# Optimization experiments

Hardware: AMD Instinct MI355X
Metric: run time of the kernel (lower is better)

The kernel has to match this reference:

```python
import jax, jax.numpy as jnp
import numpy as np

ALPHA, GAMMA = 0.25, 2.0
LOC_CW, CLS_CW, OBJ_CW = 1.0, 0.25, 0.1
LOC_W, CLS_W, OBJ_W = 1.0, 1.0, 1.0
B, K, N, C, D = 128, 2048, 4, 64, 3


def _lsa_rows(cost):
    """Hungarian (Kuhn-Munkres with potentials). cost: [n,m], n<=m.
    Returns col assigned to each row (same optimum as scipy.linear_sum_assignment)."""
    cost = np.asarray(cost, dtype=np.float64)
    n, m = cost.shape
    u = np.zeros(n + 1); v = np.zeros(m + 1)
    p = np.zeros(m + 1, dtype=np.int64)
    way = np.zeros(m + 1, dtype=np.int64)
    for i in range(1, n + 1):
        p[0] = i; j0 = 0
        minv = np.full(m + 1, np.inf)
        used = np.zeros(m + 1, dtype=bool)
        while True:
            used[j0] = True
            i0 = p[j0]
            cur = cost[i0 - 1] - u[i0] - v[1:]
            mv = minv[1:]; wy = way[1:]
            free = ~used[1:]
            upd = free & (cur < mv)
            mv[upd] = cur[upd]; wy[upd] = j0
            jrel = np.where(free)[0]
            j1 = jrel[np.argmin(mv[jrel])] + 1
            delta = mv[j1 - 1]
            uj = np.where(used)[0]
            u[p[uj]] += delta
            v[uj] -= delta
            mv[free] -= delta
            j0 = j1
            if p[j0] == 0:
                break
        while j0:
            j1 = way[j0]; p[j0] = p[j1]; j0 = j1
    col_of_row = np.full(n, -1, dtype=np.int64)
    for j in range(1, m + 1):
        if p[j] > 0:
            col_of_row[p[j] - 1] = j - 1
    return col_of_row


def focal_bce(logits, targets, alpha=ALPHA, gamma=GAMMA):
    p = jax.nn.sigmoid(logits)
    # stable BCE-with-logits
    ce = jnp.maximum(logits, 0.0) - logits * targets + jnp.log1p(jnp.exp(-jnp.abs(logits)))
    p_t = p * targets + (1.0 - p) * (1.0 - targets)
    alpha_t = alpha * targets + (1.0 - alpha) * (1.0 - targets)
    return alpha_t * ce * (1.0 - p_t) ** gamma


def _match(loc_out, obj_logit, cls_logit, gt_loc, gt_cls):
    """Hungarian matching (detached, matches torch no_grad block). Returns pred_idx [B,N];
    gt index n is matched to prediction pred_idx[b,n]."""
    eps = 1e-8
    vp = loc_out / jnp.clip(jnp.linalg.norm(loc_out, axis=-1, keepdims=True), eps)
    vt = gt_loc / jnp.clip(jnp.linalg.norm(gt_loc, axis=-1, keepdims=True), eps)
    cos = jnp.clip(jnp.einsum('bkd,bnd->bkn', vp, vt), -1.0 + 1e-6, 1.0 - 1e-6)
    loc_cost = jnp.arccos(cos) / jnp.pi  # [B,K,N]
    # cls cost: focal BCE summed over POSITIVE classes only / pos_count.
    # focal(x, t=1) = alpha * softplus(-x) * (1 - sigmoid(x))**gamma  -> einsum with one-hot gts
    focal_pos = ALPHA * jax.nn.softplus(-cls_logit) * (1.0 - jax.nn.sigmoid(cls_logit)) ** GAMMA  # [B,K,C]
    pos_cnt = jnp.maximum(gt_cls.sum(-1), 1.0)  # [B,N]
    cls_cost = jnp.einsum('bkc,bnc->bkn', focal_pos, gt_cls) / pos_cnt[:, None, :]
    obj_cost = -jax.nn.sigmoid(obj_logit)[:, :, None]  # [B,K,1]
    total = LOC_CW * loc_cost + CLS_CW * cls_cost + OBJ_CW * obj_cost  # [B,K,N]
    total_np = np.asarray(jax.device_get(total))
    # transpose to [N,K] so rows (gt) <= cols (preds)
    pred_idx = np.stack([_lsa_rows(total_np[b].T) for b in range(total_np.shape[0])])
    return jnp.asarray(pred_idx)  # [B,N] int


def _losses(loc_out, obj_logit, cls_logit, gt_loc, gt_cls, pred_idx):
    b, k = loc_out.shape[0], loc_out.shape[1]
    mp_loc = jnp.take_along_axis(loc_out, pred_idx[:, :, None], axis=1)  # [B,N,D]
    mp_cls = jnp.take_along_axis(cls_logit, pred_idx[:, :, None], axis=1)  # [B,N,C]
    # loc criterion = MSE; per-sample mean then /B == global mean (all samples have N>0)
    loc_loss = jnp.mean((mp_loc - gt_loc) ** 2)
    cls_loss = jnp.mean(focal_bce(mp_cls, gt_cls))
    obj_target = jnp.zeros((b, k), dtype=obj_logit.dtype).at[jnp.arange(b)[:, None], pred_idx].set(1.0)
    obj_ce = jnp.maximum(obj_logit, 0.0) - obj_logit * obj_target + jnp.log1p(jnp.exp(-jnp.abs(obj_logit)))
    obj_loss = jnp.mean(obj_ce)
    return LOC_W * loc_loss + CLS_W * cls_loss + OBJ_W * obj_loss


def setup_inputs() -> dict:
    key = jax.random.key(0)
    k1, k2, k3, k4, k5 = jax.random.split(key, 5)
    loc_out = jax.random.normal(k1, (B, K, D), dtype=jnp.float32)
    obj_logit = jax.random.normal(k2, (B, K), dtype=jnp.float32)
    cls_logit = jax.random.normal(k3, (B, K, C), dtype=jnp.float32)
    gt_loc = jax.random.normal(k4, (B, N, D), dtype=jnp.float32)
    cls_idx = jax.random.randint(k5, (B, N), 0, C)
    gt_cls = jax.nn.one_hot(cls_idx, C, dtype=jnp.float32)
    return {'loc_out': loc_out, 'obj_logit': obj_logit, 'cls_logit': cls_logit,
            'gt_loc': gt_loc, 'gt_cls': gt_cls}


def reference(loc_out, obj_logit, cls_logit, gt_loc, gt_cls):
    pred_idx = _match(loc_out, obj_logit, cls_logit, gt_loc, gt_cls)
    return _losses(loc_out, obj_logit, cls_logit, gt_loc, gt_cls, pred_idx)
```

## Files before the change

### kernel.cpp

```cpp
#include <hip/hip_runtime.h>
#include <math.h>
#include <limits.h>

#define BB 128
#define KK 2048
#define NN 4
#define CC 64
#define DD 3
#define SL 8
#define KS (KK/SL)
#define THREADS 256

#define OFF_CVAL 0
#define OFF_CIDX (BB*SL*NN*NN)
#define OFF_OBJ  (2*BB*SL*NN*NN)
#define OFF_PART (OFF_OBJ + BB*SL)

__device__ __forceinline__ float acospi_fast(float x) {
    float ax = fabsf(x);
    float p = ((-0.0187293f*ax + 0.0742610f)*ax - 0.2121144f)*ax + 1.5707288f;
    float r = sqrtf(1.f - ax) * p;
    r = (x >= 0.f) ? r : 3.14159274f - r;
    return r * 0.31830988618379067f;
}

__global__ void __launch_bounds__(THREADS)
crit_cost(const float* __restrict__ loc_out, const float* __restrict__ obj_logit,
          const float* __restrict__ cls_logit, const float* __restrict__ gt_loc,
          const float* __restrict__ gt_cls, float* __restrict__ ws)
{
    __shared__ float cost[NN][KS];
    __shared__ float obj_s[4];

    const int sl  = blockIdx.x;
    const int b   = blockIdx.y;
    const int tid = threadIdx.x;
    const int w   = tid >> 6, lane = tid & 63;
    const int k   = sl*KS + tid;

    const float* lp = loc_out + ((size_t)b*KK + k)*DD;
    float l0 = lp[0], l1 = lp[1], l2 = lp[2];
    float x  = obj_logit[b*KK + k];

    int   cls[NN]; float posin[NN];
    #pragma unroll
    for (int n = 0; n < NN; ++n) {
        float v = gt_cls[(b*NN+n)*CC + lane];
        unsigned long long m = __ballot(v > 0.5f);
        cls[n]   = __ffsll((unsigned long long)m) - 1;
        posin[n] = 1.f / fmaxf((float)__popcll(m), 1.f);
    }

    float z[NN];
    #pragma unroll
    for (int n = 0; n < NN; ++n)
        z[n] = cls_logit[((size_t)b*KK + k)*CC + cls[n]];

    float vt[NN][DD];
    #pragma unroll
    for (int n = 0; n < NN; ++n) {
        float g0 = gt_loc[(b*NN+n)*DD+0];
        float g1 = gt_loc[(b*NN+n)*DD+1];
        float g2 = gt_loc[(b*NN+n)*DD+2];
        float gin = 1.f / fmaxf(sqrtf(g0*g0 + g1*g1 + g2*g2), 1e-8f);
        vt[n][0] = g0*gin; vt[n][1] = g1*gin; vt[n][2] = g2*gin;
    }

    float inv = 1.f / fmaxf(sqrtf(l0*l0 + l1*l1 + l2*l2), 1e-8f);
    float v0 = l0*inv, v1 = l1*inv, v2 = l2*inv;
    float obj_base = fmaxf(x, 0.f) + log1pf(expf(-fabsf(x)));
    float oc = -0.1f / (1.f + __expf(-x));
    #pragma unroll
    for (int n = 0; n < NN; ++n) {
        float cosv = v0*vt[n][0] + v1*vt[n][1] + v2*vt[n][2];
        cosv = fminf(fmaxf(cosv, -1.f + 1e-6f), 1.f - 1e-6f);
        float loc_c = acospi_fast(cosv);
        float zz = z[n];
        float e  = __expf(-fabsf(zz));
        float lg = __logf(1.f + e);
        float sp = (zz >= 0.f) ? lg : (lg - zz);
        float r1 = 1.f / (1.f + e);
        float sn = (zz >= 0.f) ? e*r1 : r1;
        float fp = 0.25f * sp * sn * sn;
        cost[n][tid] = loc_c + 0.25f*fp*posin[n] + oc;
    }

    float osum = obj_base;
    #pragma unroll
    for (int off = 32; off > 0; off >>= 1) osum += __shfl_xor(osum, off, 64);
    if (lane == 0) obj_s[w] = osum;
    __syncthreads();

    float vv[4]; int gi[4];
    #pragma unroll
    for (int j = 0; j < 4; ++j) {
        vv[j] = cost[w][lane + 64*j];
        gi[j] = sl*KS + lane + 64*j;
    }
    float cr_val[NN]; int cr_idx[NN];
    #pragma unroll
    for (int r = 0; r < NN; ++r) {
        float bv = vv[0]; int bi = gi[0];
        #pragma unroll
        for (int j = 1; j < 4; ++j)
            if (vv[j] < bv || (vv[j] == bv && gi[j] < bi)) { bv = vv[j]; bi = gi[j]; }
        #pragma unroll
        for (int off = 32; off > 0; off >>= 1) {
            float ov = __shfl_xor(bv, off, 64);
            int   oi = __shfl_xor(bi, off, 64);
            if (ov < bv || (ov == bv && oi < bi)) { bv = ov; bi = oi; }
        }
        cr_val[r] = bv; cr_idx[r] = bi;
        #pragma unroll
        for (int j = 0; j < 4; ++j) if (gi[j] == bi) vv[j] = INFINITY;
    }
    if (lane == 0) {
        int base = ((b*SL + sl)*NN + w)*NN;
        int* wsi = (int*)ws;
        #pragma unroll
        for (int r = 0; r < NN; ++r) {
            ws[OFF_CVAL + base + r]  = cr_val[r];
            wsi[OFF_CIDX + base + r] = cr_idx[r];
        }
    }
    if (tid == 0)
        ws[OFF_OBJ + b*SL + sl] = obj_s[0] + obj_s[1] + obj_s[2] + obj_s[3];
}

__global__ void __launch_bounds__(THREADS)
crit_match(const float* __restrict__ loc_out, const float* __restrict__ obj_logit,
           const float* __restrict__ cls_logit, const float* __restrict__ gt_loc,
           const float* __restrict__ gt_cls, float* __restrict__ ws)
{
    __shared__ float cand_val[NN][NN];
    __shared__ int   cand_idx[NN][NN];
    __shared__ int   s_pred[NN];
    __shared__ float s_best[4];
    __shared__ int   s_bestc[4];
    __shared__ float red[4];

    const int b = blockIdx.x, tid = threadIdx.x;
    const int w = tid >> 6, lane = tid & 63;
    const int* wsi = (const int*)ws;

    {
        float v = INFINITY; int idx = INT_MAX;
        if (lane < SL*NN) {
            int sl = lane >> 2, r = lane & 3;
            int base = ((b*SL + sl)*NN + w)*NN + r;
            v   = ws[OFF_CVAL + base];
            idx = wsi[OFF_CIDX + base];
        }
        #pragma unroll
        for (int r = 0; r < NN; ++r) {
            float bv = v; int bi = idx;
            #pragma unroll
            for (int off = 32; off > 0; off >>= 1) {
                float ov = __shfl_xor(bv, off, 64);
                int   oi = __shfl_xor(bi, off, 64);
                if (ov < bv || (ov == bv && oi < bi)) { bv = ov; bi = oi; }
            }
            if (lane == 0) { cand_val[w][r] = bv; cand_idx[w][r] = bi; }
            if (idx == bi) v = INFINITY;
        }
    }
    __syncthreads();

    {
        int a0 = (tid >> 6) & 3, a1 = (tid >> 4) & 3, a2 = (tid >> 2) & 3, a3 = tid & 3;
        int c0 = cand_idx[0][a0], c1 = cand_idx[1][a1];
        int c2 = cand_idx[2][a2], c3 = cand_idx[3][a3];
        bool valid = (c0!=c1) & (c0!=c2) & (c0!=c3) & (c1!=c2) & (c1!=c3) & (c2!=c3);
        float t = cand_val[0][a0] + cand_val[1][a1] + cand_val[2][a2] + cand_val[3][a3];
        float bv = valid ? t : INFINITY;
        int   bc = tid;
        #pragma unroll
        for (int off = 32; off > 0; off >>= 1) {
            float ov = __shfl_xor(bv, off, 64);
            int   oc = __shfl_xor(bc, off, 64);
            if (ov < bv || (ov == bv && oc < bc)) { bv = ov; bc = oc; }
        }
        if (lane == 0) { s_best[w] = bv; s_bestc[w] = bc; }
    }
    __syncthreads();

    if (tid == 0) {
        float bv = s_best[0]; int bc = s_bestc[0];
        for (int i = 1; i < 4; ++i)
            if (s_best[i] < bv || (s_best[i] == bv && s_bestc[i] < bc)) { bv = s_best[i]; bc = s_bestc[i]; }
        int a0 = (bc >> 6) & 3, a1 = (bc >> 4) & 3, a2 = (bc >> 2) & 3, a3 = bc & 3;
        s_pred[0] = cand_idx[0][a0]; s_pred[1] = cand_idx[1][a1];
        s_pred[2] = cand_idx[2][a2]; s_pred[3] = cand_idx[3][a3];

        float om = 0.f;
        for (int sl = 0; sl < SL; ++sl) om += ws[OFF_OBJ + b*SL + sl];
        for (int n = 0; n < NN; ++n) om -= obj_logit[b*KK + s_pred[n]];
        ws[OFF_PART + b*3 + 2] = om;

        float s = 0.f;
        for (int n = 0; n < NN; ++n)
            for (int d = 0; d < DD; ++d) {
                float diff = loc_out[((size_t)b*KK + s_pred[n])*DD + d] - gt_loc[(b*NN+n)*DD + d];
                s += diff*diff;
            }
        ws[OFF_PART + b*3 + 0] = s;
    }
    __syncthreads();

    {
        int n = w, c = lane;
        float zz = cls_logit[((size_t)b*KK + s_pred[n])*CC + c];
        float tgt = gt_cls[(b*NN+n)*CC + c];
        float p  = 1.f / (1.f + expf(-zz));
        float ce = fmaxf(zz, 0.f) - zz*tgt + log1pf(expf(-fabsf(zz)));
        float pt = p*tgt + (1.f-p)*(1.f-tgt);
        float at = 0.25f*tgt + 0.75f*(1.f-tgt);
        float om1 = 1.f - pt;
        float r = at * ce * om1 * om1;
        #pragma unroll
        for (int off = 32; off > 0; off >>= 1) r += __shfl_xor(r, off, 64);
        if (lane == 0) red[n] = r;
    }
    __syncthreads();
    if (tid == 0) ws[OFF_PART + b*3 + 1] = red[0] + red[1] + red[2] + red[3];
}

__global__ void __launch_bounds__(BB)
crit_final(const float* __restrict__ ws, float* __restrict__ out)
{
    __shared__ float s2[3][2];
    int t = threadIdx.x;
    int w = t >> 6, lane = t & 63;
    float a = ws[OFF_PART + t*3+0];
    float b = ws[OFF_PART + t*3+1];
    float c = ws[OFF_PART + t*3+2];
    #pragma unroll
    for (int off = 32; off > 0; off >>= 1) {
        a += __shfl_xor(a, off, 64);
        b += __shfl_xor(b, off, 64);
        c += __shfl_xor(c, off, 64);
    }
    if (lane == 0) { s2[0][w] = a; s2[1][w] = b; s2[2][w] = c; }
    __syncthreads();
    if (t == 0) {
        out[0] = (s2[0][0]+s2[0][1]) / (float)(BB*NN*DD)
               + (s2[1][0]+s2[1][1]) / (float)(BB*NN*CC)
               + (s2[2][0]+s2[2][1]) / (float)(BB*KK);
    }
}

extern "C" void kernel_launch(void* const* d_in, const int* in_sizes, int n_in,
                              void* d_out, int out_size, void* d_ws, size_t ws_size,
                              hipStream_t stream) {
    const float* loc_out   = (const float*)d_in[0];
    const float* obj_logit = (const float*)d_in[1];
    const float* cls_logit = (const float*)d_in[2];
    const float* gt_loc    = (const float*)d_in[3];
    const float* gt_cls    = (const float*)d_in[4];
    float* ws  = (float*)d_ws;
    float* out = (float*)d_out;

    hipLaunchKernelGGL(crit_cost, dim3(SL, BB), dim3(THREADS), 0, stream,
                       loc_out, obj_logit, cls_logit, gt_loc, gt_cls, ws);
    hipLaunchKernelGGL(crit_match, dim3(BB), dim3(THREADS), 0, stream,
                       loc_out, obj_logit, cls_logit, gt_loc, gt_cls, ws);
    hipLaunchKernelGGL(crit_final, dim3(1), dim3(BB), 0, stream, ws, out);
}
```

Baseline: 28.39 us.

## Fuse cost and match kernels into one per-batch block kernel

```diff
diff --git a/kernel.cpp b/kernel.cpp
--- a/kernel.cpp
+++ b/kernel.cpp
@@ -7,14 +7,10 @@
 #define NN 4
 #define CC 64
 #define DD 3
-#define SL 8
-#define KS (KK/SL)
-#define THREADS 256
-
-#define OFF_CVAL 0
-#define OFF_CIDX (BB*SL*NN*NN)
-#define OFF_OBJ  (2*BB*SL*NN*NN)
-#define OFF_PART (OFF_OBJ + BB*SL)
+#define TA 512
+#define KPT (KK/TA)
+#define NW (TA/64)
+
 
 __device__ __forceinline__ float acospi_fast(float x) {
     float ax = fabsf(x);
@@ -24,37 +20,43 @@
     return r * 0.31830988618379067f;
 }
 
-__global__ void __launch_bounds__(THREADS)
-crit_cost(const float* __restrict__ loc_out, const float* __restrict__ obj_logit,
-          const float* __restrict__ cls_logit, const float* __restrict__ gt_loc,
-          const float* __restrict__ gt_cls, float* __restrict__ ws)
+__device__ __forceinline__ float cls_term_fast(float zz, float posin) {
+    float e  = __expf(-fabsf(zz));
+    float lg = __logf(1.f + e);
+    float sp = (zz >= 0.f) ? lg : (lg - zz);
+    float r1 = 1.f / (1.f + e);
+    float sn = (zz >= 0.f) ? e*r1 : r1;
+    float fp = 0.25f * sp * sn * sn;
+    return 0.25f * fp * posin;
+}
+
+__global__ void __launch_bounds__(TA)
+crit_all(const float* __restrict__ loc_out, const float* __restrict__ obj_logit,
+         const float* __restrict__ cls_logit, const float* __restrict__ gt_loc,
+         const float* __restrict__ gt_cls, float* __restrict__ ws)
 {
-    __shared__ float cost[NN][KS];
-    __shared__ float obj_s[4];
-
-    const int sl  = blockIdx.x;
-    const int b   = blockIdx.y;
+    __shared__ float wv_val[NW][NN][4];
+    __shared__ int   wv_idx[NW][NN][4];
+    __shared__ float obj_s[NW];
+    __shared__ float cand_val[NN][NN];
+    __shared__ int   cand_idx[NN][NN];
+    __shared__ int   s_pred[NN];
+    __shared__ float s_best[4];
+    __shared__ int   s_bestc[4];
+    __shared__ float red[4];
+
+    const int b   = blockIdx.x;
     const int tid = threadIdx.x;
     const int w   = tid >> 6, lane = tid & 63;
-    const int k   = sl*KS + tid;
-
-    const float* lp = loc_out + ((size_t)b*KK + k)*DD;
-    float l0 = lp[0], l1 = lp[1], l2 = lp[2];
-    float x  = obj_logit[b*KK + k];
 
     int   cls[NN]; float posin[NN];
     #pragma unroll
     for (int n = 0; n < NN; ++n) {
         float v = gt_cls[(b*NN+n)*CC + lane];
         unsigned long long m = __ballot(v > 0.5f);
-        cls[n]   = __ffsll((unsigned long long)m) - 1;
+        cls[n]   = __ffsll(m) - 1;
         posin[n] = 1.f / fmaxf((float)__popcll(m), 1.f);
     }
-
-    float z[NN];
-    #pragma unroll
-    for (int n = 0; n < NN; ++n)
-        z[n] = cls_logit[((size_t)b*KK + k)*CC + cls[n]];
 
     float vt[NN][DD];
     #pragma unroll
@@ -66,93 +68,63 @@
         vt[n][0] = g0*gin; vt[n][1] = g1*gin; vt[n][2] = g2*gin;
     }
 
-    float inv = 1.f / fmaxf(sqrtf(l0*l0 + l1*l1 + l2*l2), 1e-8f);
-    float v0 = l0*inv, v1 = l1*inv, v2 = l2*inv;
-    float obj_base = fmaxf(x, 0.f) + log1pf(expf(-fabsf(x)));
-    float oc = -0.1f / (1.f + __expf(-x));
+    float cost[KPT][NN];
+    float obj_base = 0.f;
+    #pragma unroll
+    for (int j = 0; j < KPT; ++j) {
+        const int k = tid + TA*j;
+        const float* lp = loc_out + ((size_t)b*KK + k)*DD;
+        float l0 = lp[0], l1 = lp[1], l2 = lp[2];
+        float x  = obj_logit[b*KK + k];
+        float inv = 1.f / fmaxf(sqrtf(l0*l0 + l1*l1 + l2*l2), 1e-8f);
+        float v0 = l0*inv, v1 = l1*inv, v2 = l2*inv;
+        obj_base += fmaxf(x, 0.f) + log1pf(expf(-fabsf(x)));
+        float oc = -0.1f / (1.f + __expf(-x));
+        #pragma unroll
+        for (int n = 0; n < NN; ++n) {
+            float cosv = v0*vt[n][0] + v1*vt[n][1] + v2*vt[n][2];
+            cosv = fminf(fmaxf(cosv, -1.f + 1e-6f), 1.f - 1e-6f);
+            float zz = cls_logit[((size_t)b*KK + k)*CC + cls[n]];
+            cost[j][n] = acospi_fast(cosv) + cls_term_fast(zz, posin[n]) + oc;
+        }
+    }
+
+    {
+        float osum = obj_base;
+        #pragma unroll
+        for (int off = 32; off > 0; off >>= 1) osum += __shfl_xor(osum, off, 64);
+        if (lane == 0) obj_s[w] = osum;
+    }
+
     #pragma unroll
     for (int n = 0; n < NN; ++n) {
-        float cosv = v0*vt[n][0] + v1*vt[n][1] + v2*vt[n][2];
-        cosv = fminf(fmaxf(cosv, -1.f + 1e-6f), 1.f - 1e-6f);
-        float loc_c = acospi_fast(cosv);
-        float zz = z[n];
-        float e  = __expf(-fabsf(zz));
-        float lg = __logf(1.f + e);
-        float sp = (zz >= 0.f) ? lg : (lg - zz);
-        float r1 = 1.f / (1.f + e);
-        float sn = (zz >= 0.f) ? e*r1 : r1;
-        float fp = 0.25f * sp * sn * sn;
-        cost[n][tid] = loc_c + 0.25f*fp*posin[n] + oc;
-    }
-
-    float osum = obj_base;
-    #pragma unroll
-    for (int off = 32; off > 0; off >>= 1) osum += __shfl_xor(osum, off, 64);
-    if (lane == 0) obj_s[w] = osum;
-    __syncthreads();
-
-    float vv[4]; int gi[4];
-    #pragma unroll
-    for (int j = 0; j < 4; ++j) {
-        vv[j] = cost[w][lane + 64*j];
-        gi[j] = sl*KS + lane + 64*j;
-    }
-    float cr_val[NN]; int cr_idx[NN];
-    #pragma unroll
-    for (int r = 0; r < NN; ++r) {
-        float bv = vv[0]; int bi = gi[0];
-        #pragma unroll
-        for (int j = 1; j < 4; ++j)
-            if (vv[j] < bv || (vv[j] == bv && gi[j] < bi)) { bv = vv[j]; bi = gi[j]; }
-        #pragma unroll
-        for (int off = 32; off > 0; off >>= 1) {
-            float ov = __shfl_xor(bv, off, 64);
-            int   oi = __shfl_xor(bi, off, 64);
-            if (ov < bv || (ov == bv && oi < bi)) { bv = ov; bi = oi; }
-        }
-        cr_val[r] = bv; cr_idx[r] = bi;
-        #pragma unroll
-        for (int j = 0; j < 4; ++j) if (gi[j] == bi) vv[j] = INFINITY;
-    }
-    if (lane == 0) {
-        int base = ((b*SL + sl)*NN + w)*NN;
-        int* wsi = (int*)ws;
-        #pragma unroll
-        for (int r = 0; r < NN; ++r) {
-            ws[OFF_CVAL + base + r]  = cr_val[r];
-            wsi[OFF_CIDX + base + r] = cr_idx[r];
-        }
-    }
-    if (tid == 0)
-        ws[OFF_OBJ + b*SL + sl] = obj_s[0] + obj_s[1] + obj_s[2] + obj_s[3];
-}
-
-__global__ void __launch_bounds__(THREADS)
-crit_match(const float* __restrict__ loc_out, const float* __restrict__ obj_logit,
-           const float* __restrict__ cls_logit, const float* __restrict__ gt_loc,
-           const float* __restrict__ gt_cls, float* __restrict__ ws)
-{
-    __shared__ float cand_val[NN][NN];
-    __shared__ int   cand_idx[NN][NN];
-    __shared__ int   s_pred[NN];
-    __shared__ float s_best[4];
-    __shared__ int   s_bestc[4];
-    __shared__ float red[4];
-
-    const int b = blockIdx.x, tid = threadIdx.x;
-    const int w = tid >> 6, lane = tid & 63;
-    const int* wsi = (const int*)ws;
-
-    {
+        float vv[KPT]; int gi[KPT];
+        #pragma unroll
+        for (int j = 0; j < KPT; ++j) { vv[j] = cost[j][n]; gi[j] = tid + TA*j; }
+        #pragma unroll
+        for (int r = 0; r < 4; ++r) {
+            float bv = vv[0]; int bi = gi[0];
+            #pragma unroll
+            for (int j = 1; j < KPT; ++j)
+                if (vv[j] < bv || (vv[j] == bv && gi[j] < bi)) { bv = vv[j]; bi = gi[j]; }
+            #pragma unroll
+            for (int off = 32; off > 0; off >>= 1) {
+                float ov = __shfl_xor(bv, off, 64);
+                int   oi = __shfl_xor(bi, off, 64);
+                if (ov < bv || (ov == bv && oi < bi)) { bv = ov; bi = oi; }
+            }
+            if (lane == 0) { wv_val[w][n][r] = bv; wv_idx[w][n][r] = bi; }
+            #pragma unroll
+            for (int j = 0; j < KPT; ++j) if (gi[j] == bi) vv[j] = INFINITY;
+        }
+    }
+    __syncthreads();
+
+    if (w < NN) {
         float v = INFINITY; int idx = INT_MAX;
-        if (lane < SL*NN) {
-            int sl = lane >> 2, r = lane & 3;
-            int base = ((b*SL + sl)*NN + w)*NN + r;
-            v   = ws[OFF_CVAL + base];
-            idx = wsi[OFF_CIDX + base];
-        }
-        #pragma unroll
-        for (int r = 0; r < NN; ++r) {
+        if (lane < NW*4) { v = wv_val[lane>>2][w][lane&3]; idx = wv_idx[lane>>2][w][lane&3]; }
+        #pragma unroll
+        for (int r = 0; r < 4; ++r) {
             float bv = v; int bi = idx;
             #pragma unroll
             for (int off = 32; off > 0; off >>= 1) {
@@ -166,7 +138,7 @@
     }
     __syncthreads();
 
-    {
+    if (tid < 256) {
         int a0 = (tid >> 6) & 3, a1 = (tid >> 4) & 3, a2 = (tid >> 2) & 3, a3 = tid & 3;
         int c0 = cand_idx[0][a0], c1 = cand_idx[1][a1];
         int c2 = cand_idx[2][a2], c3 = cand_idx[3][a3];
@@ -193,9 +165,9 @@
         s_pred[2] = cand_idx[2][a2]; s_pred[3] = cand_idx[3][a3];
 
         float om = 0.f;
-        for (int sl = 0; sl < SL; ++sl) om += ws[OFF_OBJ + b*SL + sl];
+        for (int i = 0; i < NW; ++i) om += obj_s[i];
         for (int n = 0; n < NN; ++n) om -= obj_logit[b*KK + s_pred[n]];
-        ws[OFF_PART + b*3 + 2] = om;
+        ws[b*3 + 2] = om;
 
         float s = 0.f;
         for (int n = 0; n < NN; ++n)
@@ -203,14 +175,14 @@
                 float diff = loc_out[((size_t)b*KK + s_pred[n])*DD + d] - gt_loc[(b*NN+n)*DD + d];
                 s += diff*diff;
             }
-        ws[OFF_PART + b*3 + 0] = s;
-    }
-    __syncthreads();
-
-    {
+        ws[b*3 + 0] = s;
+    }
+    __syncthreads();
+
+    if (w < NN) {
         int n = w, c = lane;
         float zz = cls_logit[((size_t)b*KK + s_pred[n])*CC + c];
-        float tgt = gt_cls[(b*NN+n)*CC + c];
+        float tgt = (c == cls[n]) ? 1.f : 0.f;
         float p  = 1.f / (1.f + expf(-zz));
         float ce = fmaxf(zz, 0.f) - zz*tgt + log1pf(expf(-fabsf(zz)));
         float pt = p*tgt + (1.f-p)*(1.f-tgt);
@@ -222,7 +194,7 @@
         if (lane == 0) red[n] = r;
     }
     __syncthreads();
-    if (tid == 0) ws[OFF_PART + b*3 + 1] = red[0] + red[1] + red[2] + red[3];
+    if (tid == 0) ws[b*3 + 1] = red[0] + red[1] + red[2] + red[3];
 }
 
 __global__ void __launch_bounds__(BB)
@@ -231,9 +203,9 @@
     __shared__ float s2[3][2];
     int t = threadIdx.x;
     int w = t >> 6, lane = t & 63;
-    float a = ws[OFF_PART + t*3+0];
-    float b = ws[OFF_PART + t*3+1];
-    float c = ws[OFF_PART + t*3+2];
+    float a = ws[t*3+0];
+    float b = ws[t*3+1];
+    float c = ws[t*3+2];
     #pragma unroll
     for (int off = 32; off > 0; off >>= 1) {
         a += __shfl_xor(a, off, 64);
@@ -260,9 +232,7 @@
     float* ws  = (float*)d_ws;
     float* out = (float*)d_out;
 
-    hipLaunchKernelGGL(crit_cost, dim3(SL, BB), dim3(THREADS), 0, stream,
-                       loc_out, obj_logit, cls_logit, gt_loc, gt_cls, ws);
-    hipLaunchKernelGGL(crit_match, dim3(BB), dim3(THREADS), 0, stream,
+    hipLaunchKernelGGL(crit_all, dim3(BB), dim3(TA), 0, stream,
                        loc_out, obj_logit, cls_logit, gt_loc, gt_cls, ws);
     hipLaunchKernelGGL(crit_final, dim3(1), dim3(BB), 0, stream, ws, out);
 }
```

New measurement: 36.78 us. 1.3x slower.
